# Kernel tuning notes

Measured on AMD Instinct MI355X. Metric: run time of the kernel, lower is better.

Reference implementation:

```python
import jax, jax.numpy as jnp
import numpy as np

MARGIN = 0.35


def setup_inputs() -> dict:
    key = jax.random.key(0)
    k1, k2 = jax.random.split(key)
    N, D = 8192, 512
    inp = jax.random.normal(k1, (N, D), dtype=jnp.float32)
    label = jax.random.randint(k2, (N,), 0, D, dtype=jnp.int64)
    return {"input": inp, "label": label}


def reference(input, label):
    N = input.shape[0]
    # Faithful to the torch code: squared-norm terms use L2-normalized input,
    # but the -2*x@x.T cross term uses the UNnormalized input (original quirk).
    x_norm = input / jnp.linalg.norm(input, axis=1, keepdims=True)
    sq = jnp.sum(x_norm * x_norm, axis=1, keepdims=True)  # [N,1]
    dist = sq + sq.T - 2.0 * (input @ input.T)            # [N,N]
    mask = label[:, None] == label[None, :]               # same-label mask
    neg_inf = jnp.array(-jnp.inf, dist.dtype)
    pos_inf = jnp.array(jnp.inf, dist.dtype)
    # hardest positive (max over same-label), hardest negative (min over diff-label)
    positive_part = jnp.max(jnp.where(mask, dist, neg_inf), axis=1)
    negative_part = jnp.min(jnp.where(mask, pos_inf, dist), axis=1)
    triplet = jnp.mean(jnp.maximum(positive_part - negative_part + MARGIN, 0.0))
    # cross entropy: input are logits, label class indices
    logz = jax.nn.logsumexp(input, axis=1)
    true_logit = jnp.take_along_axis(input, label[:, None].astype(jnp.int32), axis=1)[:, 0]
    ce = jnp.mean(logz - true_logit)
    return triplet + ce
```

## Files before the change

### kernel.cpp

```cpp
#include <hip/hip_runtime.h>
#include <hip/hip_bf16.h>
#include <stdint.h>

#define N_ROWS 8192
#define DIM 512
#define NLAB 512
#define MARGIN_F 0.35f
#define NBLK 64
#define NPURE 1953
#define NDIAG 127
#define NTILE (NPURE + NDIAG)
#define ROWSTAT_BLOCKS (N_ROWS / 4)

typedef __attribute__((ext_vector_type(4))) float floatx4;
typedef __attribute__((ext_vector_type(8))) int intx8;

__device__ __forceinline__ unsigned enc_f(float f) {
    unsigned u = __float_as_uint(f);
    return (u & 0x80000000u) ? ~u : (u | 0x80000000u);
}
__device__ __forceinline__ float dec_f(unsigned e) {
    unsigned u = (e & 0x80000000u) ? (e ^ 0x80000000u) : ~e;
    return __uint_as_float(u);
}

__device__ __forceinline__ void load_lds16(const void* g, void* l) {
    __builtin_amdgcn_global_load_lds((__attribute__((address_space(1))) void*)(void*)g,
                                     (__attribute__((address_space(3))) void*)l, 16, 0, 0);
}

__global__ __launch_bounds__(512) void histscan_kernel(const int* __restrict__ label,
                                                       int* __restrict__ offsetArr,
                                                       int* __restrict__ cnt,
                                                       float* __restrict__ out) {
    __shared__ int h[NLAB];
    __shared__ int sc[NLAB];
    int t = threadIdx.x;
    h[t] = 0;
    __syncthreads();
    for (int i = t; i < N_ROWS; i += 512) atomicAdd(&h[label[i]], 1);
    __syncthreads();
    int v = h[t];
    sc[t] = v;
    __syncthreads();
    for (int d = 1; d < NLAB; d <<= 1) {
        int add = (t >= d) ? sc[t - d] : 0;
        __syncthreads();
        sc[t] += add;
        __syncthreads();
    }
    offsetArr[t] = sc[t] - v;
    cnt[t] = 0;
    if (t == 0) out[0] = 0.f;
}

__global__ __launch_bounds__(256) void rowstats_kernel(const float* __restrict__ x,
                                                       const int* __restrict__ label,
                                                       const int* __restrict__ offsetArr,
                                                       int* __restrict__ cnt,
                                                       unsigned char* __restrict__ a8,
                                                       int* __restrict__ sortedLabel,
                                                       float* __restrict__ cePartial,
                                                       unsigned* __restrict__ minEnc,
                                                       unsigned* __restrict__ maxEnc) {
    int gid = blockIdx.x * 256 + threadIdx.x;
    if (gid < N_ROWS) { minEnc[gid] = 0xFFFFFFFFu; maxEnc[gid] = 0u; }

    int w = threadIdx.x >> 6;
    int row = blockIdx.x * 4 + w;
    int l = threadIdx.x & 63;
    const float* xr = x + (size_t)row * DIM;
    float4 v0 = ((const float4*)xr)[2 * l];
    float4 v1 = ((const float4*)xr)[2 * l + 1];
    float vals[8] = {v0.x, v0.y, v0.z, v0.w, v1.x, v1.y, v1.z, v1.w};

    float mx = vals[0];
#pragma unroll
    for (int i = 1; i < 8; i++) mx = fmaxf(mx, vals[i]);
#pragma unroll
    for (int s = 1; s < 64; s <<= 1) mx = fmaxf(mx, __shfl_xor(mx, s, 64));

    float se = 0.f;
#pragma unroll
    for (int i = 0; i < 8; i++) se += expf(vals[i] - mx);
#pragma unroll
    for (int s = 1; s < 64; s <<= 1) se += __shfl_xor(se, s, 64);

    int pos = 0;
    if (l == 0) {
        int lab = label[row];
        pos = offsetArr[lab] + atomicAdd(&cnt[lab], 1);
        sortedLabel[pos] = lab;
    }
    pos = __shfl(pos, 0, 64);

    int w0 = __builtin_amdgcn_cvt_pk_fp8_f32(vals[0], vals[1], 0, false);
    w0 = __builtin_amdgcn_cvt_pk_fp8_f32(vals[2], vals[3], w0, true);
    int w1 = __builtin_amdgcn_cvt_pk_fp8_f32(vals[4], vals[5], 0, false);
    w1 = __builtin_amdgcn_cvt_pk_fp8_f32(vals[6], vals[7], w1, true);
    ((uint2*)(a8 + (size_t)pos * DIM))[l] = make_uint2((unsigned)w0, (unsigned)w1);

    __shared__ float wsum[4];
    if (l == 0) {
        float tl = xr[label[row]];
        wsum[w] = mx + logf(se) - tl;
    }
    __syncthreads();
    if (threadIdx.x == 0)
        cePartial[blockIdx.x] = wsum[0] + wsum[1] + wsum[2] + wsum[3];
}

__global__ __launch_bounds__(256, 3) void gemm_kernel(const unsigned char* __restrict__ A,
                                                      const int* __restrict__ sortedLabel,
                                                      unsigned* __restrict__ minEnc,
                                                      unsigned* __restrict__ maxEnc) {
    __shared__ unsigned char As[128 * 128];
    __shared__ unsigned char Bs[128 * 128];
    __shared__ float redA[128][2], redB[128][2];

    int b = blockIdx.x;
    bool diag = (b < NDIAG);
    int bi, bj;
    if (diag) {
        bi = (b < 64) ? b : (b - 63);
        bj = (b < 64) ? b : (b - 64);
    } else {
        int p = b - NDIAG;
        int ci = (int)((sqrtf(8.0f * (float)p + 1.0f) - 1.0f) * 0.5f);
        while ((ci + 1) * (ci + 2) / 2 <= p) ci++;
        while (ci * (ci + 1) / 2 > p) ci--;
        bj = p - ci * (ci + 1) / 2;
        bi = ci + 2;
    }
    int ibase = bi * 128, jbase = bj * 128;

    int t = threadIdx.x;
    int w = t >> 6, l = t & 63;
    int wm = w >> 1, wn = w & 1;
    int q = l >> 4, lm = l & 15;

    floatx4 acc[4][4];
#pragma unroll
    for (int a = 0; a < 4; a++)
#pragma unroll
        for (int c = 0; c < 4; c++) acc[a][c] = (floatx4)0.f;

    int s_r = t >> 3;
    int s_c = ((t & 7) ^ (s_r & 7));

    for (int kk = 0; kk < 4; kk++) {
        int k0 = kk * 128;
#pragma unroll
        for (int i2 = 0; i2 < 4; i2++) {
            int r = i2 * 32 + s_r;
            int slot = (i2 * 256 + t) * 16;
            load_lds16(A + (size_t)(ibase + r) * DIM + k0 + s_c * 16, As + slot);
            load_lds16(A + (size_t)(jbase + r) * DIM + k0 + s_c * 16, Bs + slot);
        }
        __syncthreads();

        intx8 bfv[4];
#pragma unroll
        for (int tn = 0; tn < 4; tn++) {
            int R = wn * 64 + tn * 16 + lm;
            const int4* rowp = (const int4*)(Bs + R * 128);
            int4 lo = rowp[(2 * q) ^ (R & 7)];
            int4 hi = rowp[(2 * q + 1) ^ (R & 7)];
            intx8 v;
            v[0] = lo.x; v[1] = lo.y; v[2] = lo.z; v[3] = lo.w;
            v[4] = hi.x; v[5] = hi.y; v[6] = hi.z; v[7] = hi.w;
            bfv[tn] = v;
        }
#pragma unroll
        for (int tm = 0; tm < 4; tm++) {
            int R = wm * 64 + tm * 16 + lm;
            const int4* rowp = (const int4*)(As + R * 128);
            int4 lo = rowp[(2 * q) ^ (R & 7)];
            int4 hi = rowp[(2 * q + 1) ^ (R & 7)];
            intx8 af;
            af[0] = lo.x; af[1] = lo.y; af[2] = lo.z; af[3] = lo.w;
            af[4] = hi.x; af[5] = hi.y; af[6] = hi.z; af[7] = hi.w;
#pragma unroll
            for (int tn = 0; tn < 4; tn++)
                acc[tm][tn] = __builtin_amdgcn_mfma_scale_f32_16x16x128_f8f6f4(
                    af, bfv[tn], acc[tm][tn], 0, 0,
                    0, 0x7F7F7F7F,
                    0, 0x7F7F7F7F);
        }
        __syncthreads();
    }

    const float INF = __builtin_inff();

    if (!diag) {
        float mxJ[4];
#pragma unroll
        for (int tn = 0; tn < 4; tn++) mxJ[tn] = -INF;
#pragma unroll
        for (int tm = 0; tm < 4; tm++) {
#pragma unroll
            for (int r = 0; r < 4; r++) {
                int row_l = wm * 64 + tm * 16 + q * 4 + r;
                float mxI = -INF;
#pragma unroll
                for (int tn = 0; tn < 4; tn++) {
                    float v = acc[tm][tn][r];
                    mxI = fmaxf(mxI, v);
                    mxJ[tn] = fmaxf(mxJ[tn], v);
                }
#pragma unroll
                for (int s = 1; s < 16; s <<= 1)
                    mxI = fmaxf(mxI, __shfl_xor(mxI, s, 64));
                if (lm == 0) redA[row_l][wn] = mxI;
            }
        }
#pragma unroll
        for (int tn = 0; tn < 4; tn++) {
#pragma unroll
            for (int s = 16; s < 64; s <<= 1)
                mxJ[tn] = fmaxf(mxJ[tn], __shfl_xor(mxJ[tn], s, 64));
            if (q == 0) redB[wn * 64 + tn * 16 + lm][wm] = mxJ[tn];
        }
        __syncthreads();
        if (t < 128) {
            atomicMax(&maxEnc[ibase + t], enc_f(fmaxf(redA[t][0], redA[t][1])));
            atomicMax(&maxEnc[jbase + t], enc_f(fmaxf(redB[t][0], redB[t][1])));
        }
    } else {
        int* labi = (int*)As;
        int* labj = labi + 128;
        float (*redImn)[2] = (float (*)[2])(labj + 128);
        float (*redJmn)[2] = redImn + 128;
        if (t < 128) labi[t] = sortedLabel[ibase + t];
        else labj[t - 128] = sortedLabel[jbase + t - 128];
        __syncthreads();

        int jlab[4];
#pragma unroll
        for (int tn = 0; tn < 4; tn++) jlab[tn] = labj[wn * 64 + tn * 16 + lm];

        float mnJ[4], mxJ[4];
#pragma unroll
        for (int tn = 0; tn < 4; tn++) { mnJ[tn] = INF; mxJ[tn] = -INF; }

#pragma unroll
        for (int tm = 0; tm < 4; tm++) {
#pragma unroll
            for (int r = 0; r < 4; r++) {
                int row_l = wm * 64 + tm * 16 + q * 4 + r;
                int il = labi[row_l];
                float mnI = INF, mxI = -INF;
#pragma unroll
                for (int tn = 0; tn < 4; tn++) {
                    float v = acc[tm][tn][r];
                    bool same = (jlab[tn] == il);
                    float vs = same ? v : INF;
                    float vd = same ? -INF : v;
                    mnI = fminf(mnI, vs);
                    mxI = fmaxf(mxI, vd);
                    mnJ[tn] = fminf(mnJ[tn], vs);
                    mxJ[tn] = fmaxf(mxJ[tn], vd);
                }
#pragma unroll
                for (int s = 1; s < 16; s <<= 1) {
                    mnI = fminf(mnI, __shfl_xor(mnI, s, 64));
                    mxI = fmaxf(mxI, __shfl_xor(mxI, s, 64));
                }
                if (lm == 0) { redImn[row_l][wn] = mnI; redA[row_l][wn] = mxI; }
            }
        }
#pragma unroll
        for (int tn = 0; tn < 4; tn++) {
#pragma unroll
            for (int s = 16; s < 64; s <<= 1) {
                mnJ[tn] = fminf(mnJ[tn], __shfl_xor(mnJ[tn], s, 64));
                mxJ[tn] = fmaxf(mxJ[tn], __shfl_xor(mxJ[tn], s, 64));
            }
            if (q == 0) {
                int col_l = wn * 64 + tn * 16 + lm;
                redJmn[col_l][wm] = mnJ[tn];
                redB[col_l][wm] = mxJ[tn];
            }
        }
        __syncthreads();
        if (t < 128) {
            atomicMin(&minEnc[ibase + t], enc_f(fminf(redImn[t][0], redImn[t][1])));
            atomicMax(&maxEnc[ibase + t], enc_f(fmaxf(redA[t][0], redA[t][1])));
            atomicMin(&minEnc[jbase + t], enc_f(fminf(redJmn[t][0], redJmn[t][1])));
            atomicMax(&maxEnc[jbase + t], enc_f(fmaxf(redB[t][0], redB[t][1])));
        }
    }
}

__global__ __launch_bounds__(256) void finalize_kernel(const unsigned* __restrict__ minEnc,
                                                       const unsigned* __restrict__ maxEnc,
                                                       const float* __restrict__ cePartial,
                                                       float* __restrict__ out) {
    int gid = blockIdx.x * 256 + threadIdx.x;
    float mn = dec_f(minEnc[gid]);
    float mxv = dec_f(maxEnc[gid]);
    float s = fmaxf(2.0f * (mxv - mn) + MARGIN_F, 0.f);
    if (gid < ROWSTAT_BLOCKS) s += cePartial[gid];
#pragma unroll
    for (int sh = 1; sh < 64; sh <<= 1) s += __shfl_xor(s, sh, 64);
    __shared__ float red[4];
    int w = threadIdx.x >> 6, l = threadIdx.x & 63;
    if (l == 0) red[w] = s;
    __syncthreads();
    if (threadIdx.x == 0)
        atomicAdd(out, (red[0] + red[1] + red[2] + red[3]) * (1.0f / (float)N_ROWS));
}

extern "C" void kernel_launch(void* const* d_in, const int* in_sizes, int n_in,
                              void* d_out, int out_size, void* d_ws, size_t ws_size,
                              hipStream_t stream) {
    const float* x = (const float*)d_in[0];
    const int* label = (const int*)d_in[1];
    float* out = (float*)d_out;

    char* ws = (char*)d_ws;
    unsigned char* a8 = (unsigned char*)ws;
    char* p = ws + (size_t)N_ROWS * DIM;
    unsigned* minEnc = (unsigned*)p;            p += N_ROWS * 4;
    unsigned* maxEnc = (unsigned*)p;            p += N_ROWS * 4;
    float* cePartial = (float*)p;               p += ROWSTAT_BLOCKS * 4;
    int* offsetArr = (int*)p;                   p += NLAB * 4;
    int* cnt = (int*)p;                         p += NLAB * 4;
    int* sortedLabel = (int*)p;                 p += N_ROWS * 4;

    histscan_kernel<<<1, 512, 0, stream>>>(label, offsetArr, cnt, out);
    rowstats_kernel<<<ROWSTAT_BLOCKS, 256, 0, stream>>>(x, label, offsetArr, cnt, a8,
                                                        sortedLabel, cePartial, minEnc, maxEnc);
    gemm_kernel<<<NTILE, 256, 0, stream>>>(a8, sortedLabel, minEnc, maxEnc);
    finalize_kernel<<<32, 256, 0, stream>>>(minEnc, maxEnc, cePartial, out);
}
```

Baseline: 110.4 us.

## Make GEMM persistent with atomic tile ticket and prefetch next tile during epilogue

Turns the GEMM into a persistent kernel with 768 workgroups. Each workgroup takes tiles from a global atomic ticket counter, which histscan now resets. The first k-slice of the next tile is loaded asynchronously into LDS while the current tile's reduction epilogue runs, and later k-slices are issued right after the previous slice's MFMAs. This is meant to hide global-to-LDS latency and the per-block launch and epilogue gaps. The cost is a dedicated LDS region for the diagonal-tile scratch arrays, which was previously aliased onto As, plus extra barriers and atomic ticket traffic.

```diff
diff --git a/kernel.cpp b/kernel.cpp
--- a/kernel.cpp
+++ b/kernel.cpp
@@ -10,6 +10,7 @@
 #define NPURE 1953
 #define NDIAG 127
 #define NTILE (NPURE + NDIAG)
+#define NWORK 768
 #define ROWSTAT_BLOCKS (N_ROWS / 4)
 
 typedef __attribute__((ext_vector_type(4))) float floatx4;
@@ -32,6 +33,7 @@
 __global__ __launch_bounds__(512) void histscan_kernel(const int* __restrict__ label,
                                                        int* __restrict__ offsetArr,
                                                        int* __restrict__ cnt,
+                                                       int* __restrict__ ticket,
                                                        float* __restrict__ out) {
     __shared__ int h[NLAB];
     __shared__ int sc[NLAB];
@@ -51,7 +53,7 @@
     }
     offsetArr[t] = sc[t] - v;
     cnt[t] = 0;
-    if (t == 0) out[0] = 0.f;
+    if (t == 0) { out[0] = 0.f; ticket[0] = 0; }
 }
 
 __global__ __launch_bounds__(256) void rowstats_kernel(const float* __restrict__ x,
@@ -112,43 +114,47 @@
 
 __global__ __launch_bounds__(256, 3) void gemm_kernel(const unsigned char* __restrict__ A,
                                                       const int* __restrict__ sortedLabel,
+                                                      int* __restrict__ ticket,
                                                       unsigned* __restrict__ minEnc,
                                                       unsigned* __restrict__ maxEnc) {
     __shared__ unsigned char As[128 * 128];
     __shared__ unsigned char Bs[128 * 128];
     __shared__ float redA[128][2], redB[128][2];
-
-    int b = blockIdx.x;
-    bool diag = (b < NDIAG);
-    int bi, bj;
-    if (diag) {
-        bi = (b < 64) ? b : (b - 63);
-        bj = (b < 64) ? b : (b - 64);
-    } else {
-        int p = b - NDIAG;
-        int ci = (int)((sqrtf(8.0f * (float)p + 1.0f) - 1.0f) * 0.5f);
-        while ((ci + 1) * (ci + 2) / 2 <= p) ci++;
-        while (ci * (ci + 1) / 2 > p) ci--;
-        bj = p - ci * (ci + 1) / 2;
-        bi = ci + 2;
-    }
-    int ibase = bi * 128, jbase = bj * 128;
+    __shared__ float redImn[128][2], redJmn[128][2];
+    __shared__ int labi[128], labj[128];
+    __shared__ int nextT;
 
     int t = threadIdx.x;
     int w = t >> 6, l = t & 63;
     int wm = w >> 1, wn = w & 1;
     int q = l >> 4, lm = l & 15;
 
-    floatx4 acc[4][4];
-#pragma unroll
-    for (int a = 0; a < 4; a++)
-#pragma unroll
-        for (int c = 0; c < 4; c++) acc[a][c] = (floatx4)0.f;
-
     int s_r = t >> 3;
     int s_c = ((t & 7) ^ (s_r & 7));
 
-    for (int kk = 0; kk < 4; kk++) {
+    if (t == 0) nextT = atomicAdd(ticket, 1);
+    __syncthreads();
+    int cur = nextT;
+    if (cur >= NTILE) return;
+
+    auto decode = [&](int b, int& ibase, int& jbase, bool& diag) {
+        diag = (b < NDIAG);
+        int bi, bj;
+        if (diag) {
+            bi = (b < 64) ? b : (b - 63);
+            bj = (b < 64) ? b : (b - 64);
+        } else {
+            int p = b - NDIAG;
+            int ci = (int)((sqrtf(8.0f * (float)p + 1.0f) - 1.0f) * 0.5f);
+            while ((ci + 1) * (ci + 2) / 2 <= p) ci++;
+            while (ci * (ci + 1) / 2 > p) ci--;
+            bj = p - ci * (ci + 1) / 2;
+            bi = ci + 2;
+        }
+        ibase = bi * 128; jbase = bj * 128;
+    };
+
+    auto stage = [&](int ibase, int jbase, int kk) {
         int k0 = kk * 128;
 #pragma unroll
         for (int i2 = 0; i2 < 4; i2++) {
@@ -157,138 +163,162 @@
             load_lds16(A + (size_t)(ibase + r) * DIM + k0 + s_c * 16, As + slot);
             load_lds16(A + (size_t)(jbase + r) * DIM + k0 + s_c * 16, Bs + slot);
         }
+    };
+
+    int ibase, jbase; bool diag;
+    decode(cur, ibase, jbase, diag);
+    stage(ibase, jbase, 0);
+
+    const float INF = __builtin_inff();
+
+    while (true) {
+        floatx4 acc[4][4];
+#pragma unroll
+        for (int a = 0; a < 4; a++)
+#pragma unroll
+            for (int c = 0; c < 4; c++) acc[a][c] = (floatx4)0.f;
+
+        for (int kk = 0; kk < 4; kk++) {
+            __syncthreads();
+
+            intx8 bfv[4];
+#pragma unroll
+            for (int tn = 0; tn < 4; tn++) {
+                int R = wn * 64 + tn * 16 + lm;
+                const int4* rowp = (const int4*)(Bs + R * 128);
+                int4 lo = rowp[(2 * q) ^ (R & 7)];
+                int4 hi = rowp[(2 * q + 1) ^ (R & 7)];
+                intx8 v;
+                v[0] = lo.x; v[1] = lo.y; v[2] = lo.z; v[3] = lo.w;
+                v[4] = hi.x; v[5] = hi.y; v[6] = hi.z; v[7] = hi.w;
+                bfv[tn] = v;
+            }
+#pragma unroll
+            for (int tm = 0; tm < 4; tm++) {
+                int R = wm * 64 + tm * 16 + lm;
+                const int4* rowp = (const int4*)(As + R * 128);
+                int4 lo = rowp[(2 * q) ^ (R & 7)];
+                int4 hi = rowp[(2 * q + 1) ^ (R & 7)];
+                intx8 af;
+                af[0] = lo.x; af[1] = lo.y; af[2] = lo.z; af[3] = lo.w;
+                af[4] = hi.x; af[5] = hi.y; af[6] = hi.z; af[7] = hi.w;
+#pragma unroll
+                for (int tn = 0; tn < 4; tn++)
+                    acc[tm][tn] = __builtin_amdgcn_mfma_scale_f32_16x16x128_f8f6f4(
+                        af, bfv[tn], acc[tm][tn], 0, 0,
+                        0, 0x7F7F7F7F, 0, 0x7F7F7F7F);
+            }
+            __syncthreads();
+            if (kk < 3) stage(ibase, jbase, kk + 1);
+        }
+
+        if (t == 0) nextT = atomicAdd(ticket, 1);
         __syncthreads();
-
-        intx8 bfv[4];
-#pragma unroll
-        for (int tn = 0; tn < 4; tn++) {
-            int R = wn * 64 + tn * 16 + lm;
-            const int4* rowp = (const int4*)(Bs + R * 128);
-            int4 lo = rowp[(2 * q) ^ (R & 7)];
-            int4 hi = rowp[(2 * q + 1) ^ (R & 7)];
-            intx8 v;
-            v[0] = lo.x; v[1] = lo.y; v[2] = lo.z; v[3] = lo.w;
-            v[4] = hi.x; v[5] = hi.y; v[6] = hi.z; v[7] = hi.w;
-            bfv[tn] = v;
-        }
-#pragma unroll
-        for (int tm = 0; tm < 4; tm++) {
-            int R = wm * 64 + tm * 16 + lm;
-            const int4* rowp = (const int4*)(As + R * 128);
-            int4 lo = rowp[(2 * q) ^ (R & 7)];
-            int4 hi = rowp[(2 * q + 1) ^ (R & 7)];
-            intx8 af;
-            af[0] = lo.x; af[1] = lo.y; af[2] = lo.z; af[3] = lo.w;
-            af[4] = hi.x; af[5] = hi.y; af[6] = hi.z; af[7] = hi.w;
-#pragma unroll
-            for (int tn = 0; tn < 4; tn++)
-                acc[tm][tn] = __builtin_amdgcn_mfma_scale_f32_16x16x128_f8f6f4(
-                    af, bfv[tn], acc[tm][tn], 0, 0,
-                    0, 0x7F7F7F7F,
-                    0, 0x7F7F7F7F);
-        }
-        __syncthreads();
-    }
-
-    const float INF = __builtin_inff();
-
-    if (!diag) {
-        float mxJ[4];
-#pragma unroll
-        for (int tn = 0; tn < 4; tn++) mxJ[tn] = -INF;
-#pragma unroll
-        for (int tm = 0; tm < 4; tm++) {
-#pragma unroll
-            for (int r = 0; r < 4; r++) {
-                int row_l = wm * 64 + tm * 16 + q * 4 + r;
-                float mxI = -INF;
-#pragma unroll
-                for (int tn = 0; tn < 4; tn++) {
-                    float v = acc[tm][tn][r];
-                    mxI = fmaxf(mxI, v);
-                    mxJ[tn] = fmaxf(mxJ[tn], v);
+        int nxt = nextT;
+        int nib = 0, njb = 0; bool ndiag = false;
+        if (nxt < NTILE) {
+            decode(nxt, nib, njb, ndiag);
+            stage(nib, njb, 0);
+        }
+        if (diag) {
+            if (t < 128) labi[t] = sortedLabel[ibase + t];
+            else labj[t - 128] = sortedLabel[jbase + t - 128];
+            __syncthreads();
+        }
+
+        if (!diag) {
+            float mxJ[4];
+#pragma unroll
+            for (int tn = 0; tn < 4; tn++) mxJ[tn] = -INF;
+#pragma unroll
+            for (int tm = 0; tm < 4; tm++) {
+#pragma unroll
+                for (int r = 0; r < 4; r++) {
+                    int row_l = wm * 64 + tm * 16 + q * 4 + r;
+                    float mxI = -INF;
+#pragma unroll
+                    for (int tn = 0; tn < 4; tn++) {
+                        float v = acc[tm][tn][r];
+                        mxI = fmaxf(mxI, v);
+                        mxJ[tn] = fmaxf(mxJ[tn], v);
+                    }
+#pragma unroll
+                    for (int s = 1; s < 16; s <<= 1)
+                        mxI = fmaxf(mxI, __shfl_xor(mxI, s, 64));
+                    if (lm == 0) redA[row_l][wn] = mxI;
                 }
-#pragma unroll
-                for (int s = 1; s < 16; s <<= 1)
-                    mxI = fmaxf(mxI, __shfl_xor(mxI, s, 64));
-                if (lm == 0) redA[row_l][wn] = mxI;
-            }
-        }
-#pragma unroll
-        for (int tn = 0; tn < 4; tn++) {
-#pragma unroll
-            for (int s = 16; s < 64; s <<= 1)
-                mxJ[tn] = fmaxf(mxJ[tn], __shfl_xor(mxJ[tn], s, 64));
-            if (q == 0) redB[wn * 64 + tn * 16 + lm][wm] = mxJ[tn];
-        }
-        __syncthreads();
-        if (t < 128) {
-            atomicMax(&maxEnc[ibase + t], enc_f(fmaxf(redA[t][0], redA[t][1])));
-            atomicMax(&maxEnc[jbase + t], enc_f(fmaxf(redB[t][0], redB[t][1])));
-        }
-    } else {
-        int* labi = (int*)As;
-        int* labj = labi + 128;
-        float (*redImn)[2] = (float (*)[2])(labj + 128);
-        float (*redJmn)[2] = redImn + 128;
-        if (t < 128) labi[t] = sortedLabel[ibase + t];
-        else labj[t - 128] = sortedLabel[jbase + t - 128];
-        __syncthreads();
-
-        int jlab[4];
-#pragma unroll
-        for (int tn = 0; tn < 4; tn++) jlab[tn] = labj[wn * 64 + tn * 16 + lm];
-
-        float mnJ[4], mxJ[4];
-#pragma unroll
-        for (int tn = 0; tn < 4; tn++) { mnJ[tn] = INF; mxJ[tn] = -INF; }
-
-#pragma unroll
-        for (int tm = 0; tm < 4; tm++) {
-#pragma unroll
-            for (int r = 0; r < 4; r++) {
-                int row_l = wm * 64 + tm * 16 + q * 4 + r;
-                int il = labi[row_l];
-                float mnI = INF, mxI = -INF;
-#pragma unroll
-                for (int tn = 0; tn < 4; tn++) {
-                    float v = acc[tm][tn][r];
-                    bool same = (jlab[tn] == il);
-                    float vs = same ? v : INF;
-                    float vd = same ? -INF : v;
-                    mnI = fminf(mnI, vs);
-                    mxI = fmaxf(mxI, vd);
-                    mnJ[tn] = fminf(mnJ[tn], vs);
-                    mxJ[tn] = fmaxf(mxJ[tn], vd);
+            }
+#pragma unroll
+            for (int tn = 0; tn < 4; tn++) {
+#pragma unroll
+                for (int s = 16; s < 64; s <<= 1)
+                    mxJ[tn] = fmaxf(mxJ[tn], __shfl_xor(mxJ[tn], s, 64));
+                if (q == 0) redB[wn * 64 + tn * 16 + lm][wm] = mxJ[tn];
+            }
+            __syncthreads();
+            if (t < 128) {
+                atomicMax(&maxEnc[ibase + t], enc_f(fmaxf(redA[t][0], redA[t][1])));
+                atomicMax(&maxEnc[jbase + t], enc_f(fmaxf(redB[t][0], redB[t][1])));
+            }
+        } else {
+            int jlab[4];
+#pragma unroll
+            for (int tn = 0; tn < 4; tn++) jlab[tn] = labj[wn * 64 + tn * 16 + lm];
+
+            float mnJ[4], mxJ[4];
+#pragma unroll
+            for (int tn = 0; tn < 4; tn++) { mnJ[tn] = INF; mxJ[tn] = -INF; }
+
+#pragma unroll
+            for (int tm = 0; tm < 4; tm++) {
+#pragma unroll
+                for (int r = 0; r < 4; r++) {
+                    int row_l = wm * 64 + tm * 16 + q * 4 + r;
+                    int il = labi[row_l];
+                    float mnI = INF, mxI = -INF;
+#pragma unroll
+                    for (int tn = 0; tn < 4; tn++) {
+                        float v = acc[tm][tn][r];
+                        bool same = (jlab[tn] == il);
+                        float vs = same ? v : INF;
+                        float vd = same ? -INF : v;
+                        mnI = fminf(mnI, vs);
+                        mxI = fmaxf(mxI, vd);
+                        mnJ[tn] = fminf(mnJ[tn], vs);
+                        mxJ[tn] = fmaxf(mxJ[tn], vd);
+                    }
+#pragma unroll
+                    for (int s = 1; s < 16; s <<= 1) {
+                        mnI = fminf(mnI, __shfl_xor(mnI, s, 64));
+                        mxI = fmaxf(mxI, __shfl_xor(mxI, s, 64));
+                    }
+                    if (lm == 0) { redImn[row_l][wn] = mnI; redA[row_l][wn] = mxI; }
                 }
-#pragma unroll
-                for (int s = 1; s < 16; s <<= 1) {
-                    mnI = fminf(mnI, __shfl_xor(mnI, s, 64));
-                    mxI = fmaxf(mxI, __shfl_xor(mxI, s, 64));
+            }
+#pragma unroll
+            for (int tn = 0; tn < 4; tn++) {
+#pragma unroll
+                for (int s = 16; s < 64; s <<= 1) {
+                    mnJ[tn] = fminf(mnJ[tn], __shfl_xor(mnJ[tn], s, 64));
+                    mxJ[tn] = fmaxf(mxJ[tn], __shfl_xor(mxJ[tn], s, 64));
                 }
-                if (lm == 0) { redImn[row_l][wn] = mnI; redA[row_l][wn] = mxI; }
-            }
-        }
-#pragma unroll
-        for (int tn = 0; tn < 4; tn++) {
-#pragma unroll
-            for (int s = 16; s < 64; s <<= 1) {
-                mnJ[tn] = fminf(mnJ[tn], __shfl_xor(mnJ[tn], s, 64));
-                mxJ[tn] = fmaxf(mxJ[tn], __shfl_xor(mxJ[tn], s, 64));
-            }
-            if (q == 0) {
-                int col_l = wn * 64 + tn * 16 + lm;
-                redJmn[col_l][wm] = mnJ[tn];
-                redB[col_l][wm] = mxJ[tn];
-            }
-        }
-        __syncthreads();
-        if (t < 128) {
-            atomicMin(&minEnc[ibase + t], enc_f(fminf(redImn[t][0], redImn[t][1])));
-            atomicMax(&maxEnc[ibase + t], enc_f(fmaxf(redA[t][0], redA[t][1])));
-            atomicMin(&minEnc[jbase + t], enc_f(fminf(redJmn[t][0], redJmn[t][1])));
-            atomicMax(&maxEnc[jbase + t], enc_f(fmaxf(redB[t][0], redB[t][1])));
-        }
+                if (q == 0) {
+                    int col_l = wn * 64 + tn * 16 + lm;
+                    redJmn[col_l][wm] = mnJ[tn];
+                    redB[col_l][wm] = mxJ[tn];
+                }
+            }
+            __syncthreads();
+            if (t < 128) {
+                atomicMin(&minEnc[ibase + t], enc_f(fminf(redImn[t][0], redImn[t][1])));
+                atomicMax(&maxEnc[ibase + t], enc_f(fmaxf(redA[t][0], redA[t][1])));
+                atomicMin(&minEnc[jbase + t], enc_f(fminf(redJmn[t][0], redJmn[t][1])));
+                atomicMax(&maxEnc[jbase + t], enc_f(fmaxf(redB[t][0], redB[t][1])));
+            }
+        }
+
+        if (nxt >= NTILE) break;
+        cur = nxt; ibase = nib; jbase = njb; diag = ndiag;
     }
 }
 
@@ -327,10 +357,11 @@
     int* offsetArr = (int*)p;                   p += NLAB * 4;
     int* cnt = (int*)p;                         p += NLAB * 4;
     int* sortedLabel = (int*)p;                 p += N_ROWS * 4;
-
-    histscan_kernel<<<1, 512, 0, stream>>>(label, offsetArr, cnt, out);
+    int* ticket = (int*)p;                      p += 4;
+
+    histscan_kernel<<<1, 512, 0, stream>>>(label, offsetArr, cnt, ticket, out);
     rowstats_kernel<<<ROWSTAT_BLOCKS, 256, 0, stream>>>(x, label, offsetArr, cnt, a8,
                                                         sortedLabel, cePartial, minEnc, maxEnc);
-    gemm_kernel<<<NTILE, 256, 0, stream>>>(a8, sortedLabel, minEnc, maxEnc);
+    gemm_kernel<<<NWORK, 256, 0, stream>>>(a8, sortedLabel, ticket, minEnc, maxEnc);
     finalize_kernel<<<32, 256, 0, stream>>>(minEnc, maxEnc, cePartial, out);
 }
```

Result: slower. 216.3 us (+95.9%).
